# Kernel optimization log

Measured on AMD Instinct MI355X. Metric: run time of the kernel, lower is better.

The kernel has to match this reference:

```python
import jax, jax.numpy as jnp
import numpy as np

B, T, H, L = 64, 512, 768, 9

def setup_inputs() -> dict:
    key = jax.random.key(0)
    ks = jax.random.split(key, 6)
    hidden = jax.random.normal(ks[0], (B, T, H), jnp.float32)
    W = jax.random.normal(ks[1], (H, L), jnp.float32) * 0.02
    b = jnp.zeros((L,), jnp.float32)
    transitions = jax.random.normal(ks[2], (L, L), jnp.float32) * 0.1
    tags = jax.random.randint(ks[3], (B, T), 0, L)
    lengths = jax.random.randint(ks[4], (B,), 1, T + 1)
    return {"hidden": hidden, "W": W, "b": b, "transitions": transitions,
            "tags": tags, "lengths": lengths}


def _crf_log_likelihood(logits, tags, lengths, transitions):
    # logits [B,T,L], tags [B,T] int, lengths [B] int
    Bq, Tq, Lq = logits.shape
    t_idx = jnp.arange(Tq)
    mask = (t_idx[None, :] < lengths[:, None]).astype(logits.dtype)  # [B,T]
    # unary (emission) score along gold path
    unary = jnp.take_along_axis(logits, tags[..., None], axis=2)[..., 0]  # [B,T]
    unary_score = jnp.sum(unary * mask, axis=1)
    # transition score between consecutive gold tags
    trans_gold = transitions[tags[:, :-1], tags[:, 1:]]  # [B,T-1]
    binary_score = jnp.sum(trans_gold * mask[:, 1:], axis=1)
    # log partition via forward algorithm (scan over time)
    def step(alpha, xs):
        logit_t, m_t = xs  # [B,L], [B]
        new = jax.nn.logsumexp(alpha[:, :, None] + transitions[None], axis=1) + logit_t
        alpha = jnp.where(m_t[:, None] > 0, new, alpha)  # carry past seq end
        return alpha, None
    xs = (jnp.swapaxes(logits[:, 1:], 0, 1), jnp.swapaxes(mask[:, 1:], 0, 1))
    alpha, _ = jax.lax.scan(step, logits[:, 0], xs)
    log_norm = jax.nn.logsumexp(alpha, axis=1)
    return unary_score + binary_score - log_norm  # [B]


def _crf_decode(logits, transitions, lengths):
    Bq, Tq, Lq = logits.shape
    t_idx = jnp.arange(Tq)
    mask = t_idx[None, :] < lengths[:, None]  # [B,T] bool
    ident = jnp.broadcast_to(jnp.arange(Lq)[None, :], (Bq, Lq))
    def fwd(state, xs):
        logit_t, m_t = xs  # [B,L], [B]
        scores = state[:, :, None] + transitions[None]  # [B,Lprev,Lcur]
        bp = jnp.argmax(scores, axis=1)                 # [B,L] backpointers
        new = jnp.max(scores, axis=1) + logit_t
        state = jnp.where(m_t[:, None], new, state)
        bp = jnp.where(m_t[:, None], bp, ident)  # pass-through past seq end
        return state, bp
    xs = (jnp.swapaxes(logits[:, 1:], 0, 1), jnp.swapaxes(mask[:, 1:], 0, 1))
    state, bps = jax.lax.scan(fwd, logits[:, 0], xs)  # bps: [T-1,B,L]
    viterbi_score = jnp.max(state, axis=1)  # [B]
    last_tag = jnp.argmax(state, axis=1)    # [B]
    def back(tag, bp):
        prev = jnp.take_along_axis(bp, tag[:, None], axis=1)[:, 0]
        return prev, tag
    first_tag, rev_tags = jax.lax.scan(back, last_tag, bps, reverse=True)
    decode = jnp.concatenate([first_tag[None], rev_tags], axis=0)  # [T,B]
    decode = jnp.swapaxes(decode, 0, 1)
    decode = jnp.where(mask, decode, 0)
    return decode, viterbi_score


def reference(hidden, W, b, transitions, tags, lengths):
    # Dense(label_size, activation='relu') on BERT sequence output
    logits = jax.nn.relu(jnp.einsum('bth,hl->btl', hidden, W) + b)  # [B,T,L]
    ll = _crf_log_likelihood(logits, tags, lengths, transitions)
    loss = -jnp.mean(ll)
    decode, _score = _crf_decode(logits, transitions, lengths)
    return loss, decode
```

## Files before the change

### kernel.cpp

```cpp
#include <hip/hip_runtime.h>
#include <hip/hip_bf16.h>

#define BB 64
#define TT 512
#define HH 768
#define LL 9
#define TS 516

#define LOG2E 1.44269504088896340736f
#define LN2   0.69314718055994530942f

#if __has_builtin(__builtin_amdgcn_logf)
#define LOG2F(x) __builtin_amdgcn_logf(x)
#else
#define LOG2F(x) __log2f(x)
#endif

__device__ __forceinline__ float rlane(float v, int i) {
    return __uint_as_float((unsigned)__builtin_amdgcn_readlane((int)__float_as_uint(v), i));
}

template<int I>
__device__ __forceinline__ float dppb(float v) {
    return __uint_as_float((unsigned)__builtin_amdgcn_mov_dpp(
        (int)__float_as_uint(v), 0x150 + I, 0xF, 0xF, false));
}

__global__ __launch_bounds__(256) void logits_kernel(
    const float* __restrict__ hidden,
    const float* __restrict__ W,
    const float* __restrict__ bias,
    float* __restrict__ logits,
    int* __restrict__ ctr)
{
    if (blockIdx.x == 0 && threadIdx.x == 0) atomicExch(ctr, 0);

    __shared__ __align__(16) float WT[LL][HH];
    __shared__ float bsh[LL];

    const int tid = threadIdx.x;
    for (int idx = tid; idx < HH * LL; idx += 256) {
        int k = idx / LL, l = idx % LL;
        WT[l][k] = W[idx];
    }
    if (tid < LL) bsh[tid] = bias[tid];
    __syncthreads();

    const int wave = tid >> 6;
    const int lane = tid & 63;
    const int grp  = lane >> 4;
    const int sl   = lane & 15;
    const long row = (long)blockIdx.x * 16 + wave * 4 + grp;
    const float* hrow = hidden + row * HH;

    float acc[LL];
#pragma unroll
    for (int l = 0; l < LL; ++l) acc[l] = 0.f;

#pragma unroll
    for (int it = 0; it < 12; ++it) {
        const int k = it * 64 + sl * 4;
        float4 h = *(const float4*)(hrow + k);
#pragma unroll
        for (int l = 0; l < LL; ++l) {
            float4 w4 = *(const float4*)(&WT[l][k]);
            acc[l] += h.x * w4.x + h.y * w4.y + h.z * w4.z + h.w * w4.w;
        }
    }

#pragma unroll
    for (int l = 0; l < LL; ++l) {
        float v = acc[l];
#pragma unroll
        for (int off = 8; off; off >>= 1) v += __shfl_xor(v, off, 64);
        acc[l] = v;
    }

    if (sl < LL) {
        float v = acc[0];
#pragma unroll
        for (int l = 1; l < LL; ++l) v = (sl == l) ? acc[l] : v;
        v += bsh[sl];
        v = v > 0.f ? v : 0.f;
        logits[row * LL + sl] = v;
    }
}

__global__ __launch_bounds__(128) void crf_kernel(
    const float* __restrict__ logits,
    const float* __restrict__ trans,
    const int*  __restrict__ tags,
    const int*  __restrict__ lengths,
    float* __restrict__ ll,
    float* __restrict__ out_loss,
    float* __restrict__ out_decode,
    int* __restrict__ ctr)
{
    const int b    = blockIdx.x;
    const int tid  = threadIdx.x;
    const int wave = tid >> 6;
    const int lane = tid & 63;

    __shared__ __align__(16) float lgT[LL][TS];
    __shared__ __align__(16) int   tg[TT];
    __shared__ float trS[LL * LL];
    __shared__ __align__(16) float trST[LL][12];
    __shared__ __align__(16) float alphaS[TT][12];
    __shared__ float score_parts[4];

    const int len = lengths[b];
    const float* lgg = logits + (size_t)b * TT * LL;
    for (int i = tid; i < (TT * LL) / 4; i += 128) {
        float4 v = ((const float4*)lgg)[i];
        int base = 4 * i;
        lgT[(base    ) % LL][(base    ) / LL] = v.x;
        lgT[(base + 1) % LL][(base + 1) / LL] = v.y;
        lgT[(base + 2) % LL][(base + 2) / LL] = v.z;
        lgT[(base + 3) % LL][(base + 3) / LL] = v.w;
    }
    {
        const int4* src = (const int4*)(tags + (size_t)b * TT);
        int4* dst = (int4*)tg;
        for (int i = tid; i < TT / 4; i += 128) dst[i] = src[i];
    }
    for (int idx = tid; idx < LL * LL; idx += 128) {
        trS[idx] = trans[idx];
        trST[idx % LL][idx / LL] = trans[idx];
    }
    __syncthreads();

    float u = 0.f, bs = 0.f;
    for (int t = tid; t < len; t += 128) u += lgT[tg[t]][t];
    for (int t = tid + 1; t < len; t += 128) bs += trS[tg[t - 1] * LL + tg[t]];
#pragma unroll
    for (int off = 32; off; off >>= 1) {
        u  += __shfl_xor(u, off, 64);
        bs += __shfl_xor(bs, off, 64);
    }
    if (lane == 0) { score_parts[wave * 2] = u; score_parts[wave * 2 + 1] = bs; }
    __syncthreads();

    const int j = (lane < LL) ? lane : (LL - 1);
    float trc[LL];
#pragma unroll
    for (int i = 0; i < LL; ++i) trc[i] = trS[i * LL + j];

    const float* rowj = &lgT[j][0];

    if (wave == 0) {
        float E0 = exp2f(trc[0] * LOG2E), E1 = exp2f(trc[1] * LOG2E);
        float E2 = exp2f(trc[2] * LOG2E), E3 = exp2f(trc[3] * LOG2E);
        float E4 = exp2f(trc[4] * LOG2E), E5 = exp2f(trc[5] * LOG2E);
        float E6 = exp2f(trc[6] * LOG2E), E7 = exp2f(trc[7] * LOG2E);
        float E8 = exp2f(trc[8] * LOG2E);

        float Mlog = 0.f;
        float P0, P1, P2, P3, P4, P5, P6, P7, P8;
        {
            float Pme = exp2f(rowj[0] * LOG2E);
            P0 = rlane(Pme, 0); P1 = rlane(Pme, 1); P2 = rlane(Pme, 2);
            P3 = rlane(Pme, 3); P4 = rlane(Pme, 4); P5 = rlane(Pme, 5);
            P6 = rlane(Pme, 6); P7 = rlane(Pme, 7); P8 = rlane(Pme, 8);
        }

#define LSTEPL(GV)                                                           \
        { float p0 = P0 * E0, p1 = P1 * E1, p2 = P2 * E2;                    \
          float p3 = P3 * E3, p4 = P4 * E4, p5 = P5 * E5;                    \
          float p6 = P6 * E6, p7 = P7 * E7, p8 = P8 * E8;                    \
          float S = (((p0 + p1) + (p2 + p3)) + ((p4 + p5) + (p6 + p7)))      \
                    + p8;                                                    \
          float Pn = S * (GV);                                               \
          P0 = rlane(Pn, 0); P1 = rlane(Pn, 1); P2 = rlane(Pn, 2);           \
          P3 = rlane(Pn, 3); P4 = rlane(Pn, 4); P5 = rlane(Pn, 5);           \
          P6 = rlane(Pn, 6); P7 = rlane(Pn, 7); P8 = rlane(Pn, 8); }

#define RENORM                                                               \
        { float mx = fmaxf(fmaxf(fmaxf(fmaxf(P0, P1), fmaxf(P2, P3)),       \
                                 fmaxf(fmaxf(P4, P5), fmaxf(P6, P7))), P8); \
          int ex = (int)((__float_as_uint(mx) >> 23) & 255u) - 127;         \
          float sc = __uint_as_float((unsigned)(127 - ex) << 23);           \
          P0 *= sc; P1 *= sc; P2 *= sc; P3 *= sc; P4 *= sc;                 \
          P5 *= sc; P6 *= sc; P7 *= sc; P8 *= sc;                           \
          Mlog += (float)ex; }

        int cb = 8;
        if (len >= 8) {
            float4 c0 = *(const float4*)(rowj);
            float4 c1 = *(const float4*)(rowj + 4);
            float g1 = exp2f(c0.y * LOG2E), g2 = exp2f(c0.z * LOG2E);
            float g3 = exp2f(c0.w * LOG2E), g4 = exp2f(c1.x * LOG2E);
            float g5 = exp2f(c1.y * LOG2E), g6 = exp2f(c1.z * LOG2E);
            float g7 = exp2f(c1.w * LOG2E);
            LSTEPL(g1) LSTEPL(g2) LSTEPL(g3)
            LSTEPL(g4) LSTEPL(g5) LSTEPL(g6) LSTEPL(g7)

            float4 n0 = *(const float4*)(rowj + 8);
            float4 n1 = *(const float4*)(rowj + 12);
            for (; cb + 8 <= len; cb += 8) {
                float4 c0b = n0; float4 c1b = n1;
                if (cb + 8 < TT) {
                    n0 = *(const float4*)(rowj + cb + 8);
                    n1 = *(const float4*)(rowj + cb + 12);
                }
                float g0 = exp2f(c0b.x * LOG2E), g1b = exp2f(c0b.y * LOG2E);
                float g2b = exp2f(c0b.z * LOG2E), g3b = exp2f(c0b.w * LOG2E);
                float g4b = exp2f(c1b.x * LOG2E), g5b = exp2f(c1b.y * LOG2E);
                float g6b = exp2f(c1b.z * LOG2E), g7b = exp2f(c1b.w * LOG2E);
                RENORM
                LSTEPL(g0)  LSTEPL(g1b) LSTEPL(g2b) LSTEPL(g3b)
                LSTEPL(g4b) LSTEPL(g5b) LSTEPL(g6b) LSTEPL(g7b)
            }
        } else {
            cb = 1;
        }
        for (int t = cb; t < len; ++t) {
            float g = exp2f(rowj[t] * LOG2E);
            LSTEPL(g)
        }
        {
            float S = (((P0 + P1) + (P2 + P3)) + ((P4 + P5) + (P6 + P7)))
                      + P8;
            float log_norm = (Mlog + LOG2F(S)) * LN2;
            if (lane == 0) {
                float unary  = score_parts[0] + score_parts[2];
                float binary = score_parts[1] + score_parts[3];
                ll[b] = unary + binary - log_norm;

                __threadfence();
                int old = atomicAdd(ctr, 1);
                if (old == BB - 1) {
                    __threadfence();
                    float s = 0.f;
                    const volatile float* llv = (const volatile float*)ll;
                    for (int i = 0; i < BB; ++i) s += llv[i];
                    out_loss[0] = -s * (1.0f / 64.0f);
                }
            }
        }
    } else {
        const int acol = (lane < LL) ? lane : 11;
        float a0, a1, a2, a3, a4, a5, a6, a7, a8;
        {
            float lg0 = rowj[0];
            alphaS[0][acol] = lg0;
            a0 = dppb<0>(lg0); a1 = dppb<1>(lg0); a2 = dppb<2>(lg0);
            a3 = dppb<3>(lg0); a4 = dppb<4>(lg0); a5 = dppb<5>(lg0);
            a6 = dppb<6>(lg0); a7 = dppb<7>(lg0); a8 = dppb<8>(lg0);
        }

#define VSTEP3(LGV, TVAL)                                                    \
        { float s0 = a0 + trc[0], s1 = a1 + trc[1];                          \
          float s2 = a2 + trc[2], s3 = a3 + trc[3];                          \
          float s4 = a4 + trc[4], s5 = a5 + trc[5];                          \
          float s6 = a6 + trc[6], s7 = a7 + trc[7];                          \
          float s8 = a8 + trc[8];                                            \
          float m012 = fmaxf(fmaxf(s0, s1), s2);                             \
          float m345 = fmaxf(fmaxf(s3, s4), s5);                             \
          float m678 = fmaxf(fmaxf(s6, s7), s8);                             \
          float bv   = fmaxf(fmaxf(m012, m345), m678);                       \
          float ns = bv + (LGV);                                             \
          alphaS[TVAL][acol] = ns;                                           \
          a0 = dppb<0>(ns); a1 = dppb<1>(ns); a2 = dppb<2>(ns);              \
          a3 = dppb<3>(ns); a4 = dppb<4>(ns); a5 = dppb<5>(ns);              \
          a6 = dppb<6>(ns); a7 = dppb<7>(ns); a8 = dppb<8>(ns); }

        int cb = 8;
        if (len >= 8) {
            float4 c0 = *(const float4*)(rowj);
            float4 c1 = *(const float4*)(rowj + 4);
            VSTEP3(c0.y, 1) VSTEP3(c0.z, 2) VSTEP3(c0.w, 3)
            VSTEP3(c1.x, 4) VSTEP3(c1.y, 5) VSTEP3(c1.z, 6) VSTEP3(c1.w, 7)

            float4 n0 = *(const float4*)(rowj + 8);
            float4 n1 = *(const float4*)(rowj + 12);
            for (; cb + 8 <= len; cb += 8) {
                float4 c0b = n0; float4 c1b = n1;
                if (cb + 8 < TT) {
                    n0 = *(const float4*)(rowj + cb + 8);
                    n1 = *(const float4*)(rowj + cb + 12);
                }
                VSTEP3(c0b.x, cb + 0) VSTEP3(c0b.y, cb + 1)
                VSTEP3(c0b.z, cb + 2) VSTEP3(c0b.w, cb + 3)
                VSTEP3(c1b.x, cb + 4) VSTEP3(c1b.y, cb + 5)
                VSTEP3(c1b.z, cb + 6) VSTEP3(c1b.w, cb + 7)
            }
        } else {
            cb = 1;
        }
        for (int t = cb; t < len; ++t) {
            float lgv = rowj[t];
            VSTEP3(lgv, t)
        }

        int last_tag;
        {
            float m012 = fmaxf(fmaxf(a0, a1), a2);
            float m345 = fmaxf(fmaxf(a3, a4), a5);
            float m678 = fmaxf(fmaxf(a6, a7), a8);
            float bv   = fmaxf(fmaxf(m012, m345), m678);
            int bi = 8;
            bi = (a7 == bv) ? 7 : bi;
            bi = (a6 == bv) ? 6 : bi;
            bi = (a5 == bv) ? 5 : bi;
            bi = (a4 == bv) ? 4 : bi;
            bi = (a3 == bv) ? 3 : bi;
            bi = (a2 == bv) ? 2 : bi;
            bi = (a1 == bv) ? 1 : bi;
            bi = (a0 == bv) ? 0 : bi;
            last_tag = __builtin_amdgcn_readfirstlane(bi);
        }

        const unsigned long long IDENT = 0x876543210ULL;
        unsigned long long f[8];
        const int t0 = lane * 8;
#pragma unroll
        for (int m2 = 0; m2 < 8; ++m2) {
            int t = t0 + m2;
            unsigned long long F = IDENT;
            if (t >= 1 && t < len) {
                float4 A0 = *(const float4*)&alphaS[t - 1][0];
                float4 A1 = *(const float4*)&alphaS[t - 1][4];
                float  A8 = alphaS[t - 1][8];
                F = 0ULL;
#pragma unroll
                for (int jj = 0; jj < LL; ++jj) {
                    float4 T0 = *(const float4*)&trST[jj][0];
                    float4 T1 = *(const float4*)&trST[jj][4];
                    float  T8 = trST[jj][8];
                    float s0 = A0.x + T0.x, s1 = A0.y + T0.y;
                    float s2 = A0.z + T0.z, s3 = A0.w + T0.w;
                    float s4 = A1.x + T1.x, s5 = A1.y + T1.y;
                    float s6 = A1.z + T1.z, s7 = A1.w + T1.w;
                    float s8 = A8 + T8;
                    float m012 = fmaxf(fmaxf(s0, s1), s2);
                    float m345 = fmaxf(fmaxf(s3, s4), s5);
                    float m678 = fmaxf(fmaxf(s6, s7), s8);
                    float bv   = fmaxf(fmaxf(m012, m345), m678);
                    int bi = 8;
                    bi = (s7 == bv) ? 7 : bi;
                    bi = (s6 == bv) ? 6 : bi;
                    bi = (s5 == bv) ? 5 : bi;
                    bi = (s4 == bv) ? 4 : bi;
                    bi = (s3 == bv) ? 3 : bi;
                    bi = (s2 == bv) ? 2 : bi;
                    bi = (s1 == bv) ? 1 : bi;
                    bi = (s0 == bv) ? 0 : bi;
                    F |= ((unsigned long long)bi) << (4 * jj);
                }
            }
            f[m2] = F;
        }

        unsigned long long h = f[7];
#pragma unroll
        for (int m2 = 6; m2 >= 0; --m2) {
            unsigned long long hn = 0ULL;
#pragma unroll
            for (int jj = 0; jj < LL; ++jj) {
                int v = (int)((h >> (4 * jj)) & 15ULL);
                int w = (int)((f[m2] >> (4 * v)) & 15ULL);
                hn |= ((unsigned long long)w) << (4 * jj);
            }
            h = hn;
        }
        const unsigned hlo = (unsigned)h, hhi = (unsigned)(h >> 32);
        int tag = last_tag;
        int entry = last_tag;
        for (int l2 = 63; l2 >= 0; --l2) {
            unsigned glo = (unsigned)__builtin_amdgcn_readlane((int)hlo, l2);
            unsigned ghi = (unsigned)__builtin_amdgcn_readlane((int)hhi, l2);
            unsigned long long g = ((unsigned long long)ghi << 32) | glo;
            if (l2 == lane) entry = tag;
            tag = (int)((g >> (4 * tag)) & 15ULL);
        }
        float* dec = out_decode + (size_t)b * TT;
        int e = entry;
        {
            int t = t0 + 7;
            dec[t] = (t < len) ? (float)e : 0.f;
        }
#pragma unroll
        for (int m2 = 7; m2 >= 1; --m2) {
            e = (int)((f[m2] >> (4 * e)) & 15ULL);
            int t = t0 + m2 - 1;
            dec[t] = (t < len) ? (float)e : 0.f;
        }
    }
}

extern "C" void kernel_launch(void* const* d_in, const int* in_sizes, int n_in,
                              void* d_out, int out_size, void* d_ws, size_t ws_size,
                              hipStream_t stream)
{
    const float* hidden  = (const float*)d_in[0];
    const float* W       = (const float*)d_in[1];
    const float* bias    = (const float*)d_in[2];
    const float* trans   = (const float*)d_in[3];
    const int*   tags    = (const int*)d_in[4];
    const int*   lengths = (const int*)d_in[5];

    float* out = (float*)d_out;
    float* logits = (float*)d_ws;
    float* ll     = logits + (size_t)BB * TT * LL;
    int*   ctr    = (int*)(ll + 64);

    logits_kernel<<<2048, 256, 0, stream>>>(hidden, W, bias, logits, ctr);
    crf_kernel<<<BB, 128, 0, stream>>>(logits, trans, tags, lengths, ll,
                                       out, out + 1, ctr);
}
```

Measured before the change: 67.48 us.

## Merge forward-sum and Viterbi recurrences into one wave using DPP broadcasts

```diff
diff --git a/kernel.cpp b/kernel.cpp
--- a/kernel.cpp
+++ b/kernel.cpp
@@ -15,10 +15,6 @@
 #else
 #define LOG2F(x) __log2f(x)
 #endif
-
-__device__ __forceinline__ float rlane(float v, int i) {
-    return __uint_as_float((unsigned)__builtin_amdgcn_readlane((int)__float_as_uint(v), i));
-}
 
 template<int I>
 __device__ __forceinline__ float dppb(float v) {
@@ -107,6 +103,7 @@
     __shared__ __align__(16) float trST[LL][12];
     __shared__ __align__(16) float alphaS[TT][12];
     __shared__ float score_parts[4];
+    __shared__ int   lt_sh;
 
     const int len = lengths[b];
     const float* lgg = logits + (size_t)b * TT * LL;
@@ -140,14 +137,16 @@
     if (lane == 0) { score_parts[wave * 2] = u; score_parts[wave * 2 + 1] = bs; }
     __syncthreads();
 
-    const int j = (lane < LL) ? lane : (LL - 1);
-    float trc[LL];
-#pragma unroll
-    for (int i = 0; i < LL; ++i) trc[i] = trS[i * LL + j];
-
-    const float* rowj = &lgT[j][0];
-
     if (wave == 0) {
+        const int sl = lane & 15;
+        const int jj = (sl < LL) ? sl : (LL - 1);
+        const int rowid = lane >> 4;
+        const int acol = (rowid == 1) ? ((sl < LL) ? sl : 11) : 11;
+        const float* rowj = &lgT[jj][0];
+
+        float trc[LL];
+#pragma unroll
+        for (int i = 0; i < LL; ++i) trc[i] = trS[i * LL + jj];
         float E0 = exp2f(trc[0] * LOG2E), E1 = exp2f(trc[1] * LOG2E);
         float E2 = exp2f(trc[2] * LOG2E), E3 = exp2f(trc[3] * LOG2E);
         float E4 = exp2f(trc[4] * LOG2E), E5 = exp2f(trc[5] * LOG2E);
@@ -156,23 +155,43 @@
 
         float Mlog = 0.f;
         float P0, P1, P2, P3, P4, P5, P6, P7, P8;
+        float a0, a1, a2, a3, a4, a5, a6, a7, a8;
         {
-            float Pme = exp2f(rowj[0] * LOG2E);
-            P0 = rlane(Pme, 0); P1 = rlane(Pme, 1); P2 = rlane(Pme, 2);
-            P3 = rlane(Pme, 3); P4 = rlane(Pme, 4); P5 = rlane(Pme, 5);
-            P6 = rlane(Pme, 6); P7 = rlane(Pme, 7); P8 = rlane(Pme, 8);
-        }
-
-#define LSTEPL(GV)                                                           \
+            float lg0 = rowj[0];
+            alphaS[0][acol] = lg0;
+            float Pme = exp2f(lg0 * LOG2E);
+            P0 = dppb<0>(Pme); P1 = dppb<1>(Pme); P2 = dppb<2>(Pme);
+            P3 = dppb<3>(Pme); P4 = dppb<4>(Pme); P5 = dppb<5>(Pme);
+            P6 = dppb<6>(Pme); P7 = dppb<7>(Pme); P8 = dppb<8>(Pme);
+            a0 = dppb<0>(lg0); a1 = dppb<1>(lg0); a2 = dppb<2>(lg0);
+            a3 = dppb<3>(lg0); a4 = dppb<4>(lg0); a5 = dppb<5>(lg0);
+            a6 = dppb<6>(lg0); a7 = dppb<7>(lg0); a8 = dppb<8>(lg0);
+        }
+
+#define MSTEP(LGV, GV, TVAL)                                                 \
         { float p0 = P0 * E0, p1 = P1 * E1, p2 = P2 * E2;                    \
           float p3 = P3 * E3, p4 = P4 * E4, p5 = P5 * E5;                    \
           float p6 = P6 * E6, p7 = P7 * E7, p8 = P8 * E8;                    \
           float S = (((p0 + p1) + (p2 + p3)) + ((p4 + p5) + (p6 + p7)))      \
                     + p8;                                                    \
           float Pn = S * (GV);                                               \
-          P0 = rlane(Pn, 0); P1 = rlane(Pn, 1); P2 = rlane(Pn, 2);           \
-          P3 = rlane(Pn, 3); P4 = rlane(Pn, 4); P5 = rlane(Pn, 5);           \
-          P6 = rlane(Pn, 6); P7 = rlane(Pn, 7); P8 = rlane(Pn, 8); }
+          float s0 = a0 + trc[0], s1 = a1 + trc[1];                          \
+          float s2 = a2 + trc[2], s3 = a3 + trc[3];                          \
+          float s4 = a4 + trc[4], s5 = a5 + trc[5];                          \
+          float s6 = a6 + trc[6], s7 = a7 + trc[7];                          \
+          float s8 = a8 + trc[8];                                            \
+          float m012 = fmaxf(fmaxf(s0, s1), s2);                             \
+          float m345 = fmaxf(fmaxf(s3, s4), s5);                             \
+          float m678 = fmaxf(fmaxf(s6, s7), s8);                             \
+          float bv   = fmaxf(fmaxf(m012, m345), m678);                       \
+          float ns = bv + (LGV);                                             \
+          alphaS[TVAL][acol] = ns;                                           \
+          P0 = dppb<0>(Pn); P1 = dppb<1>(Pn); P2 = dppb<2>(Pn);              \
+          P3 = dppb<3>(Pn); P4 = dppb<4>(Pn); P5 = dppb<5>(Pn);              \
+          P6 = dppb<6>(Pn); P7 = dppb<7>(Pn); P8 = dppb<8>(Pn);              \
+          a0 = dppb<0>(ns); a1 = dppb<1>(ns); a2 = dppb<2>(ns);              \
+          a3 = dppb<3>(ns); a4 = dppb<4>(ns); a5 = dppb<5>(ns);              \
+          a6 = dppb<6>(ns); a7 = dppb<7>(ns); a8 = dppb<8>(ns); }
 
 #define RENORM                                                               \
         { float mx = fmaxf(fmaxf(fmaxf(fmaxf(P0, P1), fmaxf(P2, P3)),       \
@@ -191,8 +210,9 @@
             float g3 = exp2f(c0.w * LOG2E), g4 = exp2f(c1.x * LOG2E);
             float g5 = exp2f(c1.y * LOG2E), g6 = exp2f(c1.z * LOG2E);
             float g7 = exp2f(c1.w * LOG2E);
-            LSTEPL(g1) LSTEPL(g2) LSTEPL(g3)
-            LSTEPL(g4) LSTEPL(g5) LSTEPL(g6) LSTEPL(g7)
+            MSTEP(c0.y, g1, 1) MSTEP(c0.z, g2, 2) MSTEP(c0.w, g3, 3)
+            MSTEP(c1.x, g4, 4) MSTEP(c1.y, g5, 5) MSTEP(c1.z, g6, 6)
+            MSTEP(c1.w, g7, 7)
 
             float4 n0 = *(const float4*)(rowj + 8);
             float4 n1 = *(const float4*)(rowj + 12);
@@ -207,16 +227,20 @@
                 float g4b = exp2f(c1b.x * LOG2E), g5b = exp2f(c1b.y * LOG2E);
                 float g6b = exp2f(c1b.z * LOG2E), g7b = exp2f(c1b.w * LOG2E);
                 RENORM
-                LSTEPL(g0)  LSTEPL(g1b) LSTEPL(g2b) LSTEPL(g3b)
-                LSTEPL(g4b) LSTEPL(g5b) LSTEPL(g6b) LSTEPL(g7b)
+                MSTEP(c0b.x, g0, cb + 0)  MSTEP(c0b.y, g1b, cb + 1)
+                MSTEP(c0b.z, g2b, cb + 2) MSTEP(c0b.w, g3b, cb + 3)
+                MSTEP(c1b.x, g4b, cb + 4) MSTEP(c1b.y, g5b, cb + 5)
+                MSTEP(c1b.z, g6b, cb + 6) MSTEP(c1b.w, g7b, cb + 7)
             }
         } else {
             cb = 1;
         }
         for (int t = cb; t < len; ++t) {
-            float g = exp2f(rowj[t] * LOG2E);
-            LSTEPL(g)
-        }
+            float lgv = rowj[t];
+            float g = exp2f(lgv * LOG2E);
+            MSTEP(lgv, g, t)
+        }
+
         {
             float S = (((P0 + P1) + (P2 + P3)) + ((P4 + P5) + (P6 + P7)))
                       + P8;
@@ -225,7 +249,6 @@
                 float unary  = score_parts[0] + score_parts[2];
                 float binary = score_parts[1] + score_parts[3];
                 ll[b] = unary + binary - log_norm;
-
                 __threadfence();
                 int old = atomicAdd(ctr, 1);
                 if (old == BB - 1) {
@@ -237,62 +260,6 @@
                 }
             }
         }
-    } else {
-        const int acol = (lane < LL) ? lane : 11;
-        float a0, a1, a2, a3, a4, a5, a6, a7, a8;
-        {
-            float lg0 = rowj[0];
-            alphaS[0][acol] = lg0;
-            a0 = dppb<0>(lg0); a1 = dppb<1>(lg0); a2 = dppb<2>(lg0);
-            a3 = dppb<3>(lg0); a4 = dppb<4>(lg0); a5 = dppb<5>(lg0);
-            a6 = dppb<6>(lg0); a7 = dppb<7>(lg0); a8 = dppb<8>(lg0);
-        }
-
-#define VSTEP3(LGV, TVAL)                                                    \
-        { float s0 = a0 + trc[0], s1 = a1 + trc[1];                          \
-          float s2 = a2 + trc[2], s3 = a3 + trc[3];                          \
-          float s4 = a4 + trc[4], s5 = a5 + trc[5];                          \
-          float s6 = a6 + trc[6], s7 = a7 + trc[7];                          \
-          float s8 = a8 + trc[8];                                            \
-          float m012 = fmaxf(fmaxf(s0, s1), s2);                             \
-          float m345 = fmaxf(fmaxf(s3, s4), s5);                             \
-          float m678 = fmaxf(fmaxf(s6, s7), s8);                             \
-          float bv   = fmaxf(fmaxf(m012, m345), m678);                       \
-          float ns = bv + (LGV);                                             \
-          alphaS[TVAL][acol] = ns;                                           \
-          a0 = dppb<0>(ns); a1 = dppb<1>(ns); a2 = dppb<2>(ns);              \
-          a3 = dppb<3>(ns); a4 = dppb<4>(ns); a5 = dppb<5>(ns);              \
-          a6 = dppb<6>(ns); a7 = dppb<7>(ns); a8 = dppb<8>(ns); }
-
-        int cb = 8;
-        if (len >= 8) {
-            float4 c0 = *(const float4*)(rowj);
-            float4 c1 = *(const float4*)(rowj + 4);
-            VSTEP3(c0.y, 1) VSTEP3(c0.z, 2) VSTEP3(c0.w, 3)
-            VSTEP3(c1.x, 4) VSTEP3(c1.y, 5) VSTEP3(c1.z, 6) VSTEP3(c1.w, 7)
-
-            float4 n0 = *(const float4*)(rowj + 8);
-            float4 n1 = *(const float4*)(rowj + 12);
-            for (; cb + 8 <= len; cb += 8) {
-                float4 c0b = n0; float4 c1b = n1;
-                if (cb + 8 < TT) {
-                    n0 = *(const float4*)(rowj + cb + 8);
-                    n1 = *(const float4*)(rowj + cb + 12);
-                }
-                VSTEP3(c0b.x, cb + 0) VSTEP3(c0b.y, cb + 1)
-                VSTEP3(c0b.z, cb + 2) VSTEP3(c0b.w, cb + 3)
-                VSTEP3(c1b.x, cb + 4) VSTEP3(c1b.y, cb + 5)
-                VSTEP3(c1b.z, cb + 6) VSTEP3(c1b.w, cb + 7)
-            }
-        } else {
-            cb = 1;
-        }
-        for (int t = cb; t < len; ++t) {
-            float lgv = rowj[t];
-            VSTEP3(lgv, t)
-        }
-
-        int last_tag;
         {
             float m012 = fmaxf(fmaxf(a0, a1), a2);
             float m345 = fmaxf(fmaxf(a3, a4), a5);
@@ -307,9 +274,13 @@
             bi = (a2 == bv) ? 2 : bi;
             bi = (a1 == bv) ? 1 : bi;
             bi = (a0 == bv) ? 0 : bi;
-            last_tag = __builtin_amdgcn_readfirstlane(bi);
-        }
-
+            if (lane == 16) lt_sh = bi;
+        }
+    }
+    __syncthreads();
+
+    if (wave == 1) {
+        const int last_tag = lt_sh;
         const unsigned long long IDENT = 0x876543210ULL;
         unsigned long long f[8];
         const int t0 = lane * 8;
@@ -323,10 +294,10 @@
                 float  A8 = alphaS[t - 1][8];
                 F = 0ULL;
 #pragma unroll
-                for (int jj = 0; jj < LL; ++jj) {
-                    float4 T0 = *(const float4*)&trST[jj][0];
-                    float4 T1 = *(const float4*)&trST[jj][4];
-                    float  T8 = trST[jj][8];
+                for (int jj2 = 0; jj2 < LL; ++jj2) {
+                    float4 T0 = *(const float4*)&trST[jj2][0];
+                    float4 T1 = *(const float4*)&trST[jj2][4];
+                    float  T8 = trST[jj2][8];
                     float s0 = A0.x + T0.x, s1 = A0.y + T0.y;
                     float s2 = A0.z + T0.z, s3 = A0.w + T0.w;
                     float s4 = A1.x + T1.x, s5 = A1.y + T1.y;
@@ -345,7 +316,7 @@
                     bi = (s2 == bv) ? 2 : bi;
                     bi = (s1 == bv) ? 1 : bi;
                     bi = (s0 == bv) ? 0 : bi;
-                    F |= ((unsigned long long)bi) << (4 * jj);
+                    F |= ((unsigned long long)bi) << (4 * jj2);
                 }
             }
             f[m2] = F;
@@ -356,10 +327,10 @@
         for (int m2 = 6; m2 >= 0; --m2) {
             unsigned long long hn = 0ULL;
 #pragma unroll
-            for (int jj = 0; jj < LL; ++jj) {
-                int v = (int)((h >> (4 * jj)) & 15ULL);
+            for (int jj2 = 0; jj2 < LL; ++jj2) {
+                int v = (int)((h >> (4 * jj2)) & 15ULL);
                 int w = (int)((f[m2] >> (4 * v)) & 15ULL);
-                hn |= ((unsigned long long)w) << (4 * jj);
+                hn |= ((unsigned long long)w) << (4 * jj2);
             }
             h = hn;
         }
```

Result: slower. 98.91 us (+46.6%).
